# Performance work log

Measured on AMD Instinct MI355X. Metric: run time of the kernel, lower is better.

The kernel has to match this reference:

```python
import jax, jax.numpy as jnp
import numpy as np

B, S, H, NH, NL, G, D, A, T = 32, 512, 512, 8, 6, 8, 256, 18, 1024
HD = H // NH


def setup_inputs() -> dict:
    key = jax.random.key(0)
    ks = jax.random.split(key, 32)
    def n(k, shape, s=0.02):
        return jax.random.normal(k, shape, jnp.float32) * s
    return {
        'game_indices': jax.random.randint(ks[0], (B,), 0, G),
        'states': jax.random.normal(ks[1], (B, S, D), jnp.float32),
        'actions': jax.random.randint(ks[2], (B, S), 0, A),
        'returns_to_go': jax.random.normal(ks[3], (B, S), jnp.float32),
        'timesteps': jax.random.randint(ks[4], (B, S), 0, T),
        'attention_mask': jnp.ones((B, S), jnp.int32),
        'game_emb': n(ks[5], (G, H)),
        'obs_W': n(ks[6], (G, D, H)),
        'obs_b': n(ks[7], (G, H)),
        'obs_ln_g': jnp.ones((G, H), jnp.float32),
        'obs_ln_b': jnp.zeros((G, H), jnp.float32),
        'act_emb': n(ks[8], (G, A, H)),
        'ret_W': n(ks[9], (H,)),
        'ret_b': n(ks[10], (H,)),
        'time_emb': n(ks[11], (T, H)),
        'Wqkv': n(ks[12], (NL, 3 * H, H)),
        'bqkv': n(ks[13], (NL, 3 * H)),
        'Wo': n(ks[14], (NL, H, H)),
        'bo': n(ks[15], (NL, H)),
        'ln1_g': jnp.ones((NL, H), jnp.float32),
        'ln1_b': jnp.zeros((NL, H), jnp.float32),
        'W1': n(ks[16], (NL, 4 * H, H)),
        'b1': n(ks[17], (NL, 4 * H)),
        'W2': n(ks[18], (NL, H, 4 * H)),
        'b2': n(ks[19], (NL, H)),
        'ln2_g': jnp.ones((NL, H), jnp.float32),
        'ln2_b': jnp.zeros((NL, H), jnp.float32),
        'sh_W': n(ks[20], (G, H, D)),
        'sh_b': n(ks[21], (G, D)),
        'ah_W': n(ks[22], (G, H, A)),
        'ah_b': n(ks[23], (G, A)),
        'rh_W': n(ks[24], (H, 1)),
        'rh_b': n(ks[25], (1,)),
    }


def _ln(x, g, b, eps=1e-5):
    m = jnp.mean(x, -1, keepdims=True)
    v = jnp.mean((x - m) ** 2, -1, keepdims=True)
    return (x - m) / jnp.sqrt(v + eps) * g + b


def reference(game_indices, states, actions, returns_to_go, timesteps, attention_mask,
              game_emb, obs_W, obs_b, obs_ln_g, obs_ln_b, act_emb, ret_W, ret_b, time_emb,
              Wqkv, bqkv, Wo, bo, ln1_g, ln1_b, W1, b1, W2, b2, ln2_g, ln2_b,
              sh_W, sh_b, ah_W, ah_b, rh_W, rh_b):
    gi = game_indices
    g_emb = game_emb[gi][:, None, :]  # [B,1,H]
    # per-game routed observation embedding: Linear -> LayerNorm -> ReLU (grouped GEMM by game)
    se = jnp.einsum('bsd,bdh->bsh', states, obs_W[gi]) + obs_b[gi][:, None, :]
    se = jax.nn.relu(_ln(se, obs_ln_g[gi][:, None, :], obs_ln_b[gi][:, None, :]))
    # per-game routed action embedding table lookup
    ae = act_emb[gi[:, None], actions]  # [B,S,H]
    re = returns_to_go[..., None] * ret_W + ret_b  # Linear(1,H)
    te = time_emb[timesteps]
    x = se + ae + re + te + g_emb
    # key padding mask (src_key_padding_mask: True where attention_mask==0)
    bias = jnp.where((attention_mask == 0)[:, None, None, :], -1e9, 0.0)  # [B,1,1,S]
    scale = 1.0 / jnp.sqrt(jnp.asarray(HD, jnp.float32))
    for l in range(NL):  # post-norm TransformerEncoderLayer, relu, dropout=0 (eval)
        qkv = jnp.einsum('bsh,oh->bso', x, Wqkv[l]) + bqkv[l]
        q, k, v = jnp.split(qkv, 3, axis=-1)
        q = q.reshape(B, S, NH, HD).transpose(0, 2, 1, 3)
        k = k.reshape(B, S, NH, HD).transpose(0, 2, 1, 3)
        v = v.reshape(B, S, NH, HD).transpose(0, 2, 1, 3)
        scores = jnp.einsum('bhqd,bhkd->bhqk', q, k) * scale + bias
        attn = jnp.einsum('bhqk,bhkd->bhqd', jax.nn.softmax(scores, -1), v)
        attn = attn.transpose(0, 2, 1, 3).reshape(B, S, H)
        attn = jnp.einsum('bsh,oh->bso', attn, Wo[l]) + bo[l]
        x = _ln(x + attn, ln1_g[l], ln1_b[l])
        ff = jax.nn.relu(jnp.einsum('bsh,fh->bsf', x, W1[l]) + b1[l])
        ff = jnp.einsum('bsf,hf->bsh', ff, W2[l]) + b2[l]
        x = _ln(x + ff, ln2_g[l], ln2_b[l])
    # per-game routed prediction heads
    state_preds = jnp.einsum('bsh,bho->bso', x, sh_W[gi]) + sh_b[gi][:, None, :]
    action_preds = jnp.einsum('bsh,bho->bso', x, ah_W[gi]) + ah_b[gi][:, None, :]
    return_preds = x @ rh_W + rh_b
    return (state_preds, action_preds, return_preds)
```

## Files before the change

### kernel.cpp

```cpp
#include <hip/hip_runtime.h>

typedef __bf16 bf16x4 __attribute__((ext_vector_type(4)));
typedef __bf16 bf16x8 __attribute__((ext_vector_type(8)));
typedef float f32x4 __attribute__((ext_vector_type(4)));
typedef int int4v __attribute__((ext_vector_type(4)));

#define C1SM  0.18033688011112042592f

typedef const __attribute__((address_space(1))) void gvoid_t;
typedef __attribute__((address_space(3))) void lvoid_t;

#define SBAR()  asm volatile("s_barrier" ::: "memory")
#define WV0()   asm volatile("s_waitcnt vmcnt(0)" ::: "memory")
#define WLG0()  asm volatile("s_waitcnt lgkmcnt(0)" ::: "memory")


__global__ void cvt_f32_bf16(const float* __restrict__ src, __bf16* __restrict__ dst, int n4)
{
    int i = blockIdx.x * blockDim.x + threadIdx.x;
    if (i >= n4) return;
    f32x4 v = *reinterpret_cast<const f32x4*>(src + (size_t)i * 4);
    bf16x4 o;
    #pragma unroll
    for (int k = 0; k < 4; ++k) o[k] = (__bf16)v[k];
    *reinterpret_cast<bf16x4*>(dst + (size_t)i * 4) = o;
}

__global__ void transpose_cvt(const float* __restrict__ src, __bf16* __restrict__ dst, int R, int C)
{
    int m = blockIdx.y;
    int n = R * C;
    int i = blockIdx.x * 256 + threadIdx.x;
    if (i >= n) return;
    int c = i / R, r = i - c * R;
    dst[(size_t)m * n + i] = (__bf16)src[(size_t)m * n + (size_t)r * C + c];
}

__global__ void transpose_f32(const float* __restrict__ src, float* __restrict__ dst, int R, int C)
{
    int m = blockIdx.y;
    int n = R * C;
    int i = blockIdx.x * 256 + threadIdx.x;
    if (i >= n) return;
    int c = i / R, r = i - c * R;
    dst[(size_t)m * n + i] = src[(size_t)m * n + (size_t)r * C + c];
}

__global__ __launch_bounds__(512, 2)
void gemm256(const __bf16* __restrict__ A, const __bf16* __restrict__ B,
             const float* __restrict__ bias, __bf16* __restrict__ C,
             int ldc, int relu, __bf16* __restrict__ vt)
{
    __shared__ __bf16 lds[65536];

    const int t = threadIdx.x;
    const int w = t >> 6, lane = t & 63;
    const int l16 = lane & 15, lk = lane >> 4;
    const int wrl = (w >> 2) * 128;
    const int wcl = (w & 3) * 64;

    const int nx = gridDim.x;
    const int nwg = nx * gridDim.y;
    int orig = blockIdx.y * nx + blockIdx.x;
    int wg = ((nwg & 7) == 0) ? ((orig & 7) * (nwg >> 3) + (orig >> 3)) : orig;
    const int bm = (wg / nx) * 256, bn = (wg % nx) * 256;

    const __bf16* Ab = A + (size_t)bm * 512;
    const __bf16* Bb = B + (size_t)bn * 512;

    f32x4 acc[8][4] = {};
    bf16x8 af[4][2], bfr[2][2];

    auto stageKt = [&](int kt) {
        const int slot = kt & 1;
        #pragma unroll
        for (int h = 0; h < 4; ++h) {
            const int m = h >> 1, hf = h & 1;
            const __bf16* src = m ? Bb : Ab;
            __bf16* lb = lds + slot * 32768 + m * 16384 + hf * 8192;
            #pragma unroll
            for (int i = 0; i < 2; ++i) {
                int u = i * 512 + t;
                int row = hf * 128 + (u >> 3);
                int ch = (u & 7) ^ (row & 7);
                const __bf16* ga = src + (size_t)row * 512 + kt * 64 + ch * 8;
                __builtin_amdgcn_global_load_lds((gvoid_t*)ga,
                    (lvoid_t*)(lb + (i * 512 + w * 64) * 8), 16, 0, 0);
            }
        }
    };
    auto ldA = [&](int slot, int mh) {
        const __bf16* la = lds + slot * 32768;
        #pragma unroll
        for (int mi = 0; mi < 4; ++mi) {
            int row = wrl + mh * 64 + mi * 16 + l16;
            #pragma unroll
            for (int ks = 0; ks < 2; ++ks) {
                int c = (ks * 4 + lk) ^ (row & 7);
                af[mi][ks] = *reinterpret_cast<const bf16x8*>(la + row * 64 + c * 8);
            }
        }
    };
    auto ldB = [&](int slot, int nh) {
        const __bf16* lb = lds + slot * 32768 + 16384;
        #pragma unroll
        for (int nf = 0; nf < 2; ++nf) {
            int row = wcl + nh * 32 + nf * 16 + l16;
            #pragma unroll
            for (int ks = 0; ks < 2; ++ks) {
                int c = (ks * 4 + lk) ^ (row & 7);
                bfr[nf][ks] = *reinterpret_cast<const bf16x8*>(lb + row * 64 + c * 8);
            }
        }
    };
    auto quad = [&](int mh, int nh) {
        __builtin_amdgcn_s_setprio(1);
        #pragma unroll
        for (int mi = 0; mi < 4; ++mi)
            #pragma unroll
            for (int nf = 0; nf < 2; ++nf)
                #pragma unroll
                for (int ks = 0; ks < 2; ++ks)
                    acc[mh * 4 + mi][nh * 2 + nf] = __builtin_amdgcn_mfma_f32_16x16x32_bf16(
                        af[mi][ks], bfr[nf][ks], acc[mh * 4 + mi][nh * 2 + nf], 0, 0, 0);
        __builtin_amdgcn_s_setprio(0);
    };

    stageKt(0);
    #pragma unroll
    for (int kt = 0; kt < 8; ++kt) {
        const int slot = kt & 1;
        WV0();
        SBAR();
        if (kt < 7) stageKt(kt + 1);
        ldA(slot, 0); ldB(slot, 0);
        SBAR(); quad(0, 0); SBAR();
        ldB(slot, 1);
        SBAR(); quad(0, 1); SBAR();
        ldA(slot, 1);
        SBAR(); quad(1, 1); SBAR();
        ldB(slot, 0);
        SBAR(); quad(1, 0); SBAR();
    }

    if (vt && bn >= 1024) {
        const int bb = bm >> 9;
        const int s0 = (bm & 511) + wrl + lk * 4;
        #pragma unroll
        for (int nf = 0; nf < 4; ++nf) {
            int c = bn + wcl + nf * 16 + l16;
            float bv = bias[c];
            int hh = (c - 1024) >> 6, d = c & 63;
            __bf16* vrow = vt + ((size_t)(bb * 8 + hh) * 64 + d) * 512;
            #pragma unroll
            for (int mf = 0; mf < 8; ++mf) {
                bf16x4 o;
                #pragma unroll
                for (int j = 0; j < 4; ++j) o[j] = (__bf16)(acc[mf][nf][j] + bv);
                *reinterpret_cast<bf16x4*>(vrow + s0 + mf * 16) = o;
            }
        }
        return;
    }

    SBAR();
    __bf16* lc = lds;
    #pragma unroll
    for (int nf = 0; nf < 4; ++nf) {
        int col = wcl + nf * 16 + l16;
        float bv = bias[bn + col];
        #pragma unroll
        for (int mf = 0; mf < 8; ++mf)
            #pragma unroll
            for (int j = 0; j < 4; ++j) {
                float v = acc[mf][nf][j] + bv;
                if (relu) v = fmaxf(v, 0.f);
                lc[(wrl + mf * 16 + lk * 4 + j) * 256 + col] = (__bf16)v;
            }
    }
    WLG0();
    SBAR();
    #pragma unroll
    for (int i = 0; i < 16; ++i) {
        int off = i * 4096 + t * 8;
        int r = off >> 8, c2 = off & 255;
        *reinterpret_cast<int4v*>(C + (size_t)(bm + r) * ldc + bn + c2) =
            *reinterpret_cast<const int4v*>(lc + off);
    }
}

__global__ __launch_bounds__(256, 4)
void gemm_bt(const __bf16* __restrict__ A, size_t strideA,
             const __bf16* __restrict__ B, size_t strideB,
             const float* __restrict__ bias, int strideBias,
             float* Cf, __bf16* Cb, size_t strideC,
             const int* __restrict__ gidx, int ldk, int Klen,
             size_t splitStride, int ldc, int relu, __bf16* __restrict__ vt)
{
    __shared__ __align__(16) char smem[32768];
    __bf16* lCb = (__bf16*)smem;
    float*  lCf = (float*)smem;

    const int z = blockIdx.z;
    const int g = gidx ? gidx[z] : 0;
    const __bf16* Ab = A + (splitStride ? (size_t)z * Klen : (size_t)z * strideA);
    const __bf16* Bb = B + (splitStride ? (size_t)z * Klen : (size_t)g * strideB);
    __bf16* CbO = Cb ? (Cb + (size_t)z * (splitStride ? splitStride : strideC)) : nullptr;
    float*  CfO = Cf ? (Cf + (size_t)z * strideC) : nullptr;
    const float* biasb = (bias && (!splitStride || z == 0)) ? bias + (size_t)g * strideBias : nullptr;

    const int nx = gridDim.x;
    const int nwg = nx * gridDim.y;
    int orig = blockIdx.y * nx + blockIdx.x;
    int wg = ((nwg & 7) == 0) ? ((orig & 7) * (nwg >> 3) + (orig >> 3)) : orig;
    const int bm = (wg / nx) * 128, bn = (wg % nx) * 128;

    const int t = threadIdx.x;
    const int w = t >> 6, lane = t & 63;
    const int wr = (w >> 1) * 64, wc = (w & 1) * 64;
    const int l16 = lane & 15, lk = lane >> 4;

    const int srow = lane >> 2;
    const int schunk = (lane & 3) ^ ((srow >> 1) & 3);
    const int ca = (lk ^ ((l16 >> 1) & 3)) * 8;

    f32x4 acc[4][4] = {};

    auto stage = [&](int buf, int kt) {
        __bf16* la = (__bf16*)(smem + buf * 16384);
        __bf16* lb = la + 4096;
        #pragma unroll
        for (int jj = 0; jj < 2; ++jj) {
            const __bf16* ga = Ab + (size_t)(bm + w * 32 + jj * 16 + srow) * ldk + kt + schunk * 8;
            __builtin_amdgcn_global_load_lds((gvoid_t*)ga, (lvoid_t*)&la[(w * 32 + jj * 16) * 32], 16, 0, 0);
            const __bf16* gb = Bb + (size_t)(bn + w * 32 + jj * 16 + srow) * ldk + kt + schunk * 8;
            __builtin_amdgcn_global_load_lds((gvoid_t*)gb, (lvoid_t*)&lb[(w * 32 + jj * 16) * 32], 16, 0, 0);
        }
    };

    stage(0, 0);
    __syncthreads();
    int cur = 0;
    for (int kt = 0; kt < Klen; kt += 32) {
        if (kt + 32 < Klen) stage(cur ^ 1, kt + 32);
        __bf16* la = (__bf16*)(smem + cur * 16384);
        __bf16* lb = la + 4096;
        bf16x8 af[4], bfr[4];
        #pragma unroll
        for (int i = 0; i < 4; ++i) {
            af[i]  = *reinterpret_cast<const bf16x8*>(&la[(wr + i * 16 + l16) * 32 + ca]);
            bfr[i] = *reinterpret_cast<const bf16x8*>(&lb[(wc + i * 16 + l16) * 32 + ca]);
        }
        #pragma unroll
        for (int mi = 0; mi < 4; ++mi)
            #pragma unroll
            for (int ni = 0; ni < 4; ++ni)
                acc[mi][ni] = __builtin_amdgcn_mfma_f32_16x16x32_bf16(af[mi], bfr[ni], acc[mi][ni], 0, 0, 0);
        __syncthreads();
        cur ^= 1;
    }

    if (vt && bn >= 1024) {
        const int bb = bm >> 9;
        const int s0 = (bm & 511) + wr + lk * 4;
        #pragma unroll
        for (int ni = 0; ni < 4; ++ni) {
            int c = bn + wc + ni * 16 + l16;
            float bv = biasb ? biasb[c] : 0.f;
            int hh = (c - 1024) >> 6, d = c & 63;
            __bf16* vrow = vt + ((size_t)(bb * 8 + hh) * 64 + d) * 512;
            #pragma unroll
            for (int mi = 0; mi < 4; ++mi) {
                bf16x4 o;
                #pragma unroll
                for (int j = 0; j < 4; ++j) o[j] = (__bf16)(acc[mi][ni][j] + bv);
                *reinterpret_cast<bf16x4*>(vrow + s0 + mi * 16) = o;
            }
        }
        return;
    }

    if (CbO) {
        #pragma unroll
        for (int ni = 0; ni < 4; ++ni) {
            int col = wc + ni * 16 + l16;
            float bv = biasb ? biasb[bn + col] : 0.f;
            #pragma unroll
            for (int mi = 0; mi < 4; ++mi)
                #pragma unroll
                for (int j = 0; j < 4; ++j) {
                    float v = acc[mi][ni][j] + bv;
                    if (relu) v = fmaxf(v, 0.f);
                    lCb[(wr + mi * 16 + lk * 4 + j) * 128 + col] = (__bf16)v;
                }
        }
        __syncthreads();
        #pragma unroll
        for (int it = 0; it < 8; ++it) {
            int off = it * 2048 + t * 8;
            int rl = off >> 7, col = off & 127;
            *reinterpret_cast<int4v*>(CbO + (size_t)(bm + rl) * ldc + bn + col) =
                *reinterpret_cast<const int4v*>(&lCb[off]);
        }
    } else {
        #pragma unroll
        for (int p = 0; p < 2; ++p) {
            if (p) __syncthreads();
            if (wr == p * 64) {
                #pragma unroll
                for (int ni = 0; ni < 4; ++ni) {
                    int col = wc + ni * 16 + l16;
                    float bv = biasb ? biasb[bn + col] : 0.f;
                    #pragma unroll
                    for (int mi = 0; mi < 4; ++mi)
                        #pragma unroll
                        for (int j = 0; j < 4; ++j) {
                            float v = acc[mi][ni][j] + bv;
                            if (relu) v = fmaxf(v, 0.f);
                            lCf[(mi * 16 + lk * 4 + j) * 128 + col] = v;
                        }
                }
            }
            __syncthreads();
            #pragma unroll
            for (int it = 0; it < 8; ++it) {
                int off = it * 1024 + t * 4;
                int rl = off >> 7, col = off & 127;
                *reinterpret_cast<f32x4*>(CfO + (size_t)(bm + p * 64 + rl) * ldc + bn + col) =
                    *reinterpret_cast<const f32x4*>(&lCf[off]);
            }
        }
    }
}

__global__ __launch_bounds__(256, 4)
void attn_fwd_c(const __bf16* __restrict__ qkv, const __bf16* __restrict__ vt,
                const int* __restrict__ mask, __bf16* __restrict__ out)
{
    __shared__ __bf16 lK[2][64 * 64];
    __shared__ __bf16 lV[2][64 * 64];
    __shared__ __bf16 lP[4][16 * 32];
    __shared__ float lM2[512];

    const int bh = blockIdx.x;
    const int b = bh >> 3, h = bh & 7;
    const int q0 = blockIdx.y * 128;
    const int t = threadIdx.x, w = t >> 6, lane = t & 63;
    const int l16 = lane & 15, lk = lane >> 4;

    const __bf16* qbase = qkv + (size_t)b * 512 * 1536 + h * 64;
    const __bf16* kbase = qbase + 512;
    const __bf16* vtb = vt + (size_t)(b * 8 + h) * 64 * 512;

    bf16x8 qfr[2][2];
    #pragma unroll
    for (int qn = 0; qn < 2; ++qn) {
        int row = q0 + w * 32 + qn * 16 + l16;
        #pragma unroll
        for (int kc = 0; kc < 2; ++kc)
            qfr[qn][kc] = *reinterpret_cast<const bf16x8*>(qbase + (size_t)row * 1536 + (kc * 4 + lk) * 8);
    }
    {
        int i0 = t * 2;
        lM2[i0]     = (mask[b * 512 + i0] == 0)     ? -2e9f : 0.f;
        lM2[i0 + 1] = (mask[b * 512 + i0 + 1] == 0) ? -2e9f : 0.f;
    }

    auto stageKV = [&](int buf, int kt) {
        #pragma unroll
        for (int r = 0; r < 2; ++r) {
            int c = r * 256 + w * 64 + lane;
            int row = c >> 3, ch = c & 7;
            const __bf16* ga = kbase + (size_t)(kt + row) * 1536 + ((ch ^ (row & 7)) * 8);
            __builtin_amdgcn_global_load_lds((gvoid_t*)ga,
                (lvoid_t*)(&lK[buf][0] + (r * 256 + w * 64) * 8), 16, 0, 0);
            const __bf16* gv = vtb + (size_t)row * 512 + kt + ((ch ^ (row & 7)) * 8);
            __builtin_amdgcn_global_load_lds((gvoid_t*)gv,
                (lvoid_t*)(&lV[buf][0] + (r * 256 + w * 64) * 8), 16, 0, 0);
        }
    };

    float m_run[2] = {-1e30f, -1e30f}, l_run[2] = {0.f, 0.f};
    f32x4 oacc[2][4] = {};
    const int xsw = ((l16 >> 1) & 3) << 1;

    stageKV(0, 0);
    __syncthreads();

    int cur = 0;
    for (int kt = 0; kt < 512; kt += 64) {
        if (kt + 64 < 512) stageKV(cur ^ 1, kt + 64);
        const __bf16* lKc = &lK[cur][0];
        const __bf16* lVc = &lV[cur][0];
        __bf16* lp = &lP[w][0];

        #pragma unroll
        for (int qn = 0; qn < 2; ++qn) {
            f32x4 sacc[4] = {};
            #pragma unroll
            for (int ni = 0; ni < 4; ++ni) {
                int krow = ni * 16 + l16;
                #pragma unroll
                for (int kc = 0; kc < 2; ++kc) {
                    bf16x8 kf = *reinterpret_cast<const bf16x8*>(&lKc[krow * 64 + (((kc * 4 + lk) ^ (krow & 7)) * 8)]);
                    sacc[ni] = __builtin_amdgcn_mfma_f32_16x16x32_bf16(kf, qfr[qn][kc], sacc[ni], 0, 0, 0);
                }
            }

            f32x4 mx4 = {-3e38f, -3e38f, -3e38f, -3e38f};
            #pragma unroll
            for (int ni = 0; ni < 4; ++ni) {
                f32x4 mkv = *reinterpret_cast<const f32x4*>(&lM2[kt + ni * 16 + lk * 4]);
                f32x4 sv;
                #pragma unroll
                for (int j = 0; j < 4; ++j) {
                    sv[j] = fmaf(sacc[ni][j], C1SM, mkv[j]);
                    mx4[j] = fmaxf(mx4[j], sv[j]);
                }
                sacc[ni] = sv;
            }
            float mx = fmaxf(fmaxf(mx4[0], mx4[1]), fmaxf(mx4[2], mx4[3]));
            mx = fmaxf(mx, __shfl_xor(mx, 16));
            mx = fmaxf(mx, __shfl_xor(mx, 32));
            bool need = mx > m_run[qn] + 11.54f;
            if (__any((int)need)) {
                float mn = fmaxf(m_run[qn], mx);
                float alpha = exp2f(m_run[qn] - mn);
                m_run[qn] = mn;
                l_run[qn] *= alpha;
                #pragma unroll
                for (int j = 0; j < 4; ++j) {
                    float aj = __shfl(alpha, lk * 4 + j);
                    #pragma unroll
                    for (int dn = 0; dn < 4; ++dn) oacc[qn][dn][j] *= aj;
                }
            }
            f32x4 ps4 = {0.f, 0.f, 0.f, 0.f};
            #pragma unroll
            for (int ni = 0; ni < 4; ++ni)
                #pragma unroll
                for (int j = 0; j < 4; ++j) {
                    float p = exp2f(sacc[ni][j] - m_run[qn]);
                    sacc[ni][j] = p;
                    ps4[j] += p;
                }
            l_run[qn] += (ps4[0] + ps4[1]) + (ps4[2] + ps4[3]);

            #pragma unroll
            for (int kc = 0; kc < 2; ++kc) {
                #pragma unroll
                for (int n2 = 0; n2 < 2; ++n2) {
                    bf16x4 o;
                    #pragma unroll
                    for (int j = 0; j < 4; ++j) o[j] = (__bf16)sacc[kc * 2 + n2][j];
                    *reinterpret_cast<bf16x4*>(&lp[l16 * 32 + ((n2 * 4 + lk) ^ xsw) * 4]) = o;
                }
                bf16x8 pf = *reinterpret_cast<const bf16x8*>(&lp[l16 * 32 + (lk ^ (xsw >> 1)) * 8]);
                #pragma unroll
                for (int dn = 0; dn < 4; ++dn) {
                    int vrow = dn * 16 + l16;
                    bf16x8 vf = *reinterpret_cast<const bf16x8*>(&lVc[vrow * 64 + (((kc * 4 + lk) ^ (vrow & 7)) * 8)]);
                    oacc[qn][dn] = __builtin_amdgcn_mfma_f32_16x16x32_bf16(pf, vf, oacc[qn][dn], 0, 0, 0);
                }
            }
        }
        __syncthreads();
        cur ^= 1;
    }

    #pragma unroll
    for (int qn = 0; qn < 2; ++qn) {
        float s = l_run[qn];
        s += __shfl_xor(s, 16);
        s += __shfl_xor(s, 32);
        float linv = 1.f / s;
        #pragma unroll
        for (int j = 0; j < 4; ++j) {
            float lj = __shfl(linv, lk * 4 + j);
            #pragma unroll
            for (int dn = 0; dn < 4; ++dn) {
                int row = q0 + w * 32 + qn * 16 + lk * 4 + j;
                int col = h * 64 + dn * 16 + l16;
                out[(size_t)(b * 512 + row) * 512 + col] = (__bf16)(oacc[qn][dn][j] * lj);
            }
        }
    }
}


__device__ __forceinline__ float wsum64(float v)
{
    #pragma unroll
    for (int d = 32; d >= 1; d >>= 1) v += __shfl_xor(v, d);
    return v;
}

__global__ __launch_bounds__(256)
void ln_fuse2(const __bf16* resid, const __bf16* __restrict__ pA,
              const __bf16* __restrict__ pB,
              const float* __restrict__ gamma, const float* __restrict__ beta,
              __bf16* xbo)
{
    int tok = blockIdx.x * 4 + (threadIdx.x >> 6);
    int lane = threadIdx.x & 63;
    size_t base = (size_t)tok * 512 + lane * 8;
    float y[8];
    {
        bf16x8 rv = *reinterpret_cast<const bf16x8*>(resid + base);
        bf16x8 pa = *reinterpret_cast<const bf16x8*>(pA + base);
        bf16x8 pb = *reinterpret_cast<const bf16x8*>(pB + base);
        #pragma unroll
        for (int i = 0; i < 8; ++i) y[i] = (float)rv[i] + (float)pa[i] + (float)pb[i];
    }
    float s = 0.f;
    #pragma unroll
    for (int i = 0; i < 8; ++i) s += y[i];
    float mean = wsum64(s) * (1.f / 512.f);
    float v = 0.f;
    #pragma unroll
    for (int i = 0; i < 8; ++i) { float d = y[i] - mean; v += d * d; }
    float rstd = rsqrtf(wsum64(v) * (1.f / 512.f) + 1e-5f);
    int hh = lane * 8;
    f32x4 g0 = *reinterpret_cast<const f32x4*>(gamma + hh);
    f32x4 g1 = *reinterpret_cast<const f32x4*>(gamma + hh + 4);
    f32x4 b0 = *reinterpret_cast<const f32x4*>(beta + hh);
    f32x4 b1 = *reinterpret_cast<const f32x4*>(beta + hh + 4);
    bf16x8 ob;
    #pragma unroll
    for (int i = 0; i < 4; ++i) {
        ob[i]     = (__bf16)((y[i] - mean) * rstd * g0[i] + b0[i]);
        ob[4 + i] = (__bf16)((y[4 + i] - mean) * rstd * g1[i] + b1[i]);
    }
    *reinterpret_cast<bf16x8*>(xbo + base) = ob;
}

__global__ __launch_bounds__(256)
void embed_fin(const __bf16* __restrict__ seraw, const int* __restrict__ gi,
               const int* __restrict__ actions, const float* __restrict__ rtg,
               const int* __restrict__ ts,
               const float* __restrict__ olg, const float* __restrict__ olb,
               const float* __restrict__ act_emb, const float* __restrict__ retW,
               const float* __restrict__ retb, const float* __restrict__ time_emb,
               const float* __restrict__ game_emb,
               __bf16* __restrict__ xbo)
{
    int tok = blockIdx.x * 4 + (threadIdx.x >> 6);
    int lane = threadIdx.x & 63;
    int b = tok >> 9;
    int g = gi[b];
    int a = actions[tok];
    int tt = ts[tok];
    float rv = rtg[tok];
    size_t base = (size_t)tok * 512 + lane * 8;
    int hh = lane * 8;

    float y[8];
    {
        bf16x8 a0 = *reinterpret_cast<const bf16x8*>(seraw + base);
        #pragma unroll
        for (int i = 0; i < 8; ++i) y[i] = (float)a0[i];
    }
    float s = 0.f;
    #pragma unroll
    for (int i = 0; i < 8; ++i) s += y[i];
    float mean = wsum64(s) * (1.f / 512.f);
    float v = 0.f;
    #pragma unroll
    for (int i = 0; i < 8; ++i) { float d = y[i] - mean; v += d * d; }
    float rstd = rsqrtf(wsum64(v) * (1.f / 512.f) + 1e-5f);

    const float* gp = olg + (size_t)g * 512 + hh;
    const float* bp = olb + (size_t)g * 512 + hh;
    const float* ap = act_emb + ((size_t)g * 18 + a) * 512 + hh;
    const float* tp = time_emb + (size_t)tt * 512 + hh;
    const float* ep = game_emb + (size_t)g * 512 + hh;
    const float* rwp = retW + hh;
    const float* rbp = retb + hh;

    bf16x8 ob;
    #pragma unroll
    for (int half = 0; half < 2; ++half) {
        f32x4 gv = *reinterpret_cast<const f32x4*>(gp + half * 4);
        f32x4 bv = *reinterpret_cast<const f32x4*>(bp + half * 4);
        f32x4 av = *reinterpret_cast<const f32x4*>(ap + half * 4);
        f32x4 tv = *reinterpret_cast<const f32x4*>(tp + half * 4);
        f32x4 ev = *reinterpret_cast<const f32x4*>(ep + half * 4);
        f32x4 rw = *reinterpret_cast<const f32x4*>(rwp + half * 4);
        f32x4 rb = *reinterpret_cast<const f32x4*>(rbp + half * 4);
        #pragma unroll
        for (int i = 0; i < 4; ++i) {
            float n = (y[half * 4 + i] - mean) * rstd * gv[i] + bv[i];
            n = fmaxf(n, 0.f);
            float o = n + av[i] + rv * rw[i] + rb[i] + tv[i] + ev[i];
            ob[half * 4 + i] = (__bf16)o;
        }
    }
    *reinterpret_cast<bf16x8*>(xbo + base) = ob;
}

__global__ __launch_bounds__(256)
void head_ar(const __bf16* __restrict__ xbv, const int* __restrict__ gi,
             const float* __restrict__ ahWt, const float* __restrict__ ah_b,
             const float* __restrict__ rhW, const float* __restrict__ rhb,
             float* __restrict__ outA, float* __restrict__ outR)
{
    int tok = blockIdx.x * 4 + (threadIdx.x >> 6);
    int lane = threadIdx.x & 63;
    int b = tok >> 9;
    int g = gi[b];
    size_t base = (size_t)tok * 512 + lane * 8;
    float x[8];
    {
        bf16x8 a0 = *reinterpret_cast<const bf16x8*>(xbv + base);
        #pragma unroll
        for (int i = 0; i < 8; ++i) x[i] = (float)a0[i];
    }
    #pragma unroll 1
    for (int a = 0; a < 18; ++a) {
        const float* wp = ahWt + ((size_t)g * 18 + a) * 512 + lane * 8;
        f32x4 w0 = *reinterpret_cast<const f32x4*>(wp);
        f32x4 w1 = *reinterpret_cast<const f32x4*>(wp + 4);
        float p = 0.f;
        #pragma unroll
        for (int i = 0; i < 4; ++i) { p += x[i] * w0[i]; p += x[4 + i] * w1[i]; }
        p = wsum64(p);
        if (lane == 0) outA[(size_t)tok * 18 + a] = p + ah_b[g * 18 + a];
    }
    {
        const float* wp = rhW + lane * 8;
        f32x4 w0 = *reinterpret_cast<const f32x4*>(wp);
        f32x4 w1 = *reinterpret_cast<const f32x4*>(wp + 4);
        float p = 0.f;
        #pragma unroll
        for (int i = 0; i < 4; ++i) { p += x[i] * w0[i]; p += x[4 + i] * w1[i]; }
        p = wsum64(p);
        if (lane == 0) outR[tok] = p + rhb[0];
    }
}


extern "C" void kernel_launch(void* const* d_in, const int* in_sizes, int n_in,
                              void* d_out, int out_size, void* d_ws, size_t ws_size,
                              hipStream_t stream)
{
    (void)in_sizes; (void)n_in; (void)out_size; (void)ws_size;

    const int*   gi       = (const int*)d_in[0];
    const float* states   = (const float*)d_in[1];
    const int*   actions  = (const int*)d_in[2];
    const float* rtg      = (const float*)d_in[3];
    const int*   ts       = (const int*)d_in[4];
    const int*   amask    = (const int*)d_in[5];
    const float* game_emb = (const float*)d_in[6];
    const float* obs_W    = (const float*)d_in[7];
    const float* obs_b    = (const float*)d_in[8];
    const float* obs_ln_g = (const float*)d_in[9];
    const float* obs_ln_b = (const float*)d_in[10];
    const float* act_emb  = (const float*)d_in[11];
    const float* ret_W    = (const float*)d_in[12];
    const float* ret_b    = (const float*)d_in[13];
    const float* time_emb = (const float*)d_in[14];
    const float* Wqkv     = (const float*)d_in[15];
    const float* bqkv     = (const float*)d_in[16];
    const float* Wo       = (const float*)d_in[17];
    const float* bo       = (const float*)d_in[18];
    const float* ln1_g    = (const float*)d_in[19];
    const float* ln1_b    = (const float*)d_in[20];
    const float* W1       = (const float*)d_in[21];
    const float* b1       = (const float*)d_in[22];
    const float* W2       = (const float*)d_in[23];
    const float* b2       = (const float*)d_in[24];
    const float* ln2_g    = (const float*)d_in[25];
    const float* ln2_b    = (const float*)d_in[26];
    const float* sh_W     = (const float*)d_in[27];
    const float* sh_b     = (const float*)d_in[28];
    const float* ah_W     = (const float*)d_in[29];
    const float* ah_b     = (const float*)d_in[30];
    const float* rh_W     = (const float*)d_in[31];
    const float* rh_b     = (const float*)d_in[32];

    char* wsb = (char*)d_ws;
    __bf16* tmp     = (__bf16*)(wsb + 0);
    __bf16* tmp2    = tmp + 8388608;
    __bf16* xb      = (__bf16*)(wsb + 33554432);
    __bf16* vT      = (__bf16*)(wsb + 67108864);
    __bf16* qkvB    = (__bf16*)(wsb + 83886080);
    __bf16* ff1B    = qkvB;
    __bf16* statesB = qkvB;
    __bf16* obswB   = (__bf16*)(wsb + 83886080 + 8388608);
    __bf16* attnB   = (__bf16*)(wsb + 150994944);
    __bf16* wqkvB   = (__bf16*)(wsb + 167772160);
    __bf16* woB     = (__bf16*)(wsb + 177209344);
    __bf16* w1B     = (__bf16*)(wsb + 180355072);
    __bf16* w2B     = (__bf16*)(wsb + 192937984);
    __bf16* shwB    = (__bf16*)(wsb + 205520896);
    float*  ahwT    = (float*)(wsb + 207618048);

    cvt_f32_bf16<<<4608, 256, 0, stream>>>(Wqkv, wqkvB, 1179648);
    cvt_f32_bf16<<<1536, 256, 0, stream>>>(Wo, woB, 393216);
    cvt_f32_bf16<<<6144, 256, 0, stream>>>(W1, w1B, 1572864);
    cvt_f32_bf16<<<6144, 256, 0, stream>>>(W2, w2B, 1572864);
    cvt_f32_bf16<<<4096, 256, 0, stream>>>(states, statesB, 1048576);
    transpose_cvt<<<dim3(512, 8), 256, 0, stream>>>(obs_W, obswB, 256, 512);
    transpose_cvt<<<dim3(512, 8), 256, 0, stream>>>(sh_W, shwB, 512, 256);
    transpose_f32<<<dim3(36, 8), 256, 0, stream>>>(ah_W, ahwT, 512, 18);

    gemm_bt<<<dim3(4, 4, 32), 256, 0, stream>>>(
        statesB, (size_t)512 * 256, obswB, (size_t)512 * 256, obs_b, 512,
        nullptr, tmp, (size_t)512 * 512, gi, 256, 256, 0, 512, 0, nullptr);
    embed_fin<<<4096, 256, 0, stream>>>(tmp, gi, actions, rtg, ts,
        obs_ln_g, obs_ln_b, act_emb, ret_W, ret_b, time_emb, game_emb, xb);

    for (int l = 0; l < 6; ++l) {
        gemm256<<<dim3(6, 64), 512, 0, stream>>>(
            xb, wqkvB + (size_t)l * 1536 * 512, bqkv + l * 1536, qkvB, 1536, 0, vT);
        attn_fwd_c<<<dim3(256, 4, 1), 256, 0, stream>>>(qkvB, vT, amask, attnB);
        gemm_bt<<<dim3(4, 128, 2), 256, 0, stream>>>(
            attnB, 0, woB + (size_t)l * 512 * 512, 0, bo + l * 512, 0,
            nullptr, tmp, 0, nullptr, 512, 256, 8388608, 512, 0, nullptr);
        ln_fuse2<<<4096, 256, 0, stream>>>(xb, tmp, tmp2, ln1_g + l * 512, ln1_b + l * 512, xb);
        gemm256<<<dim3(8, 64), 512, 0, stream>>>(
            xb, w1B + (size_t)l * 2048 * 512, b1 + l * 2048, ff1B, 2048, 1, nullptr);
        gemm_bt<<<dim3(4, 128, 2), 256, 0, stream>>>(
            ff1B, 0, w2B + (size_t)l * 512 * 2048, 0, b2 + l * 512, 0,
            nullptr, tmp, 0, nullptr, 2048, 1024, 8388608, 512, 0, nullptr);
        ln_fuse2<<<4096, 256, 0, stream>>>(xb, tmp, tmp2, ln2_g + l * 512, ln2_b + l * 512, xb);
    }

    gemm_bt<<<dim3(2, 4, 32), 256, 0, stream>>>(
        xb, (size_t)512 * 512, shwB, (size_t)256 * 512, sh_b, 256,
        (float*)d_out, nullptr, (size_t)512 * 256, gi, 512, 512, 0, 256, 0, nullptr);
    head_ar<<<4096, 256, 0, stream>>>(xb, gi, ahwT, ah_b, rh_W, rh_b,
        (float*)d_out + 4194304, (float*)d_out + 4489216);
}
```

Before: 1.394 ms.

## Generalize gemm256 for split-K, deeper prefetch, and route FFN2 through it

The 256x256 LDS-staged GEMM now takes a K stride, a K-tile count and a split-K stride. Its main loop prefetches two K-tiles ahead, waiting on a partial vmcnt instead of draining all loads. The second FFN GEMM (K=2048) now runs on this kernel with a 2-way split-K writing bf16 partials, replacing the smaller-tile gemm_bt. This aims to overlap loads with MFMA work and use the faster tile kernel for FFN2. The loop is no longer fully unrolled, and the split-K partials may go through ln_fuse2 in bf16 instead of the layout it expected before.

After: 1.402 ms. No clear change (+0.6%).

```diff
diff --git a/kernel.cpp b/kernel.cpp
--- a/kernel.cpp
+++ b/kernel.cpp
@@ -11,7 +11,6 @@
 typedef __attribute__((address_space(3))) void lvoid_t;
 
 #define SBAR()  asm volatile("s_barrier" ::: "memory")
-#define WV0()   asm volatile("s_waitcnt vmcnt(0)" ::: "memory")
 #define WLG0()  asm volatile("s_waitcnt lgkmcnt(0)" ::: "memory")
 
 
@@ -49,7 +48,8 @@
 __global__ __launch_bounds__(512, 2)
 void gemm256(const __bf16* __restrict__ A, const __bf16* __restrict__ B,
              const float* __restrict__ bias, __bf16* __restrict__ C,
-             int ldc, int relu, __bf16* __restrict__ vt)
+             int ldc, int relu, __bf16* __restrict__ vt,
+             int ldk, int nkt, size_t splitStride)
 {
     __shared__ __bf16 lds[65536];
 
@@ -59,14 +59,19 @@
     const int wrl = (w >> 2) * 128;
     const int wcl = (w & 3) * 64;
 
+    const int z = blockIdx.z;
+    const int koff = z * nkt * 64;
+    __bf16* Cb = C + (size_t)z * splitStride;
+    const bool dobias = (splitStride == 0) || (z == 0);
+
     const int nx = gridDim.x;
     const int nwg = nx * gridDim.y;
     int orig = blockIdx.y * nx + blockIdx.x;
     int wg = ((nwg & 7) == 0) ? ((orig & 7) * (nwg >> 3) + (orig >> 3)) : orig;
     const int bm = (wg / nx) * 256, bn = (wg % nx) * 256;
 
-    const __bf16* Ab = A + (size_t)bm * 512;
-    const __bf16* Bb = B + (size_t)bn * 512;
+    const __bf16* Ab = A + (size_t)bm * ldk + koff;
+    const __bf16* Bb = B + (size_t)bn * ldk + koff;
 
     f32x4 acc[8][4] = {};
     bf16x8 af[4][2], bfr[2][2];
@@ -83,7 +88,7 @@
                 int u = i * 512 + t;
                 int row = hf * 128 + (u >> 3);
                 int ch = (u & 7) ^ (row & 7);
-                const __bf16* ga = src + (size_t)row * 512 + kt * 64 + ch * 8;
+                const __bf16* ga = src + (size_t)row * ldk + kt * 64 + ch * 8;
                 __builtin_amdgcn_global_load_lds((gvoid_t*)ga,
                     (lvoid_t*)(lb + (i * 512 + w * 64) * 8), 16, 0, 0);
             }
@@ -127,12 +132,12 @@
     };
 
     stageKt(0);
-    #pragma unroll
-    for (int kt = 0; kt < 8; ++kt) {
+    if (nkt > 1) stageKt(1);
+    for (int kt = 0; kt < nkt; ++kt) {
         const int slot = kt & 1;
-        WV0();
+        if (kt + 1 < nkt) asm volatile("s_waitcnt vmcnt(8)" ::: "memory");
+        else              asm volatile("s_waitcnt vmcnt(0)" ::: "memory");
         SBAR();
-        if (kt < 7) stageKt(kt + 1);
         ldA(slot, 0); ldB(slot, 0);
         SBAR(); quad(0, 0); SBAR();
         ldB(slot, 1);
@@ -141,6 +146,7 @@
         SBAR(); quad(1, 1); SBAR();
         ldB(slot, 0);
         SBAR(); quad(1, 0); SBAR();
+        if (kt + 2 < nkt) stageKt(kt + 2);
     }
 
     if (vt && bn >= 1024) {
@@ -168,7 +174,7 @@
     #pragma unroll
     for (int nf = 0; nf < 4; ++nf) {
         int col = wcl + nf * 16 + l16;
-        float bv = bias[bn + col];
+        float bv = dobias ? bias[bn + col] : 0.f;
         #pragma unroll
         for (int mf = 0; mf < 8; ++mf)
             #pragma unroll
@@ -184,7 +190,7 @@
     for (int i = 0; i < 16; ++i) {
         int off = i * 4096 + t * 8;
         int r = off >> 8, c2 = off & 255;
-        *reinterpret_cast<int4v*>(C + (size_t)(bm + r) * ldc + bn + c2) =
+        *reinterpret_cast<int4v*>(Cb + (size_t)(bm + r) * ldc + bn + c2) =
             *reinterpret_cast<const int4v*>(lc + off);
     }
 }
@@ -712,18 +718,20 @@
         obs_ln_g, obs_ln_b, act_emb, ret_W, ret_b, time_emb, game_emb, xb);
 
     for (int l = 0; l < 6; ++l) {
-        gemm256<<<dim3(6, 64), 512, 0, stream>>>(
-            xb, wqkvB + (size_t)l * 1536 * 512, bqkv + l * 1536, qkvB, 1536, 0, vT);
+        gemm256<<<dim3(6, 64, 1), 512, 0, stream>>>(
+            xb, wqkvB + (size_t)l * 1536 * 512, bqkv + l * 1536, qkvB, 1536, 0, vT,
+            512, 8, 0);
         attn_fwd_c<<<dim3(256, 4, 1), 256, 0, stream>>>(qkvB, vT, amask, attnB);
         gemm_bt<<<dim3(4, 128, 2), 256, 0, stream>>>(
             attnB, 0, woB + (size_t)l * 512 * 512, 0, bo + l * 512, 0,
             nullptr, tmp, 0, nullptr, 512, 256, 8388608, 512, 0, nullptr);
         ln_fuse2<<<4096, 256, 0, stream>>>(xb, tmp, tmp2, ln1_g + l * 512, ln1_b + l * 512, xb);
-        gemm256<<<dim3(8, 64), 512, 0, stream>>>(
-            xb, w1B + (size_t)l * 2048 * 512, b1 + l * 2048, ff1B, 2048, 1, nullptr);
-        gemm_bt<<<dim3(4, 128, 2), 256, 0, stream>>>(
-            ff1B, 0, w2B + (size_t)l * 512 * 2048, 0, b2 + l * 512, 0,
-            nullptr, tmp, 0, nullptr, 2048, 1024, 8388608, 512, 0, nullptr);
+        gemm256<<<dim3(8, 64, 1), 512, 0, stream>>>(
+            xb, w1B + (size_t)l * 2048 * 512, b1 + l * 2048, ff1B, 2048, 1, nullptr,
+            512, 8, 0);
+        gemm256<<<dim3(2, 64, 2), 512, 0, stream>>>(
+            ff1B, w2B + (size_t)l * 512 * 2048, b2 + l * 512, tmp, 512, 0, nullptr,
+            2048, 16, 8388608);
         ln_fuse2<<<4096, 256, 0, stream>>>(xb, tmp, tmp2, ln2_g + l * 512, ln2_b + l * 512, xb);
     }
 
```
